# Performance work log

Measured on AMD Instinct MI355X. Metric: run time of the kernel, lower is better.

Reference implementation:

```python
import jax, jax.numpy as jnp
import numpy as np

HEADS = 16
D_MODEL = 1024
HEAD_DIM = D_MODEL // HEADS
NEG = -1e15


def setup_inputs() -> dict:
    key = jax.random.key(0)
    ks = jax.random.split(key, 13)
    B, L = 2, 2048
    scale = 1.0 / np.sqrt(D_MODEL)
    inp = {
        'q': jax.random.normal(ks[0], (B, L, D_MODEL), jnp.float32),
        'k': jax.random.normal(ks[1], (B, L, D_MODEL), jnp.float32),
        'v': jax.random.normal(ks[2], (B, L, D_MODEL), jnp.float32),
        'mask': jax.random.randint(ks[3], (B, 1, 1, L), 0, 2, jnp.int32),
        'Wq': jax.random.normal(ks[4], (D_MODEL, D_MODEL), jnp.float32) * scale,
        'bq': jax.random.normal(ks[5], (D_MODEL,), jnp.float32) * scale,
        'Wk': jax.random.normal(ks[6], (D_MODEL, D_MODEL), jnp.float32) * scale,
        'bk': jax.random.normal(ks[7], (D_MODEL,), jnp.float32) * scale,
        'Wv': jax.random.normal(ks[8], (D_MODEL, D_MODEL), jnp.float32) * scale,
        'bv': jax.random.normal(ks[9], (D_MODEL,), jnp.float32) * scale,
        'Wo': jax.random.normal(ks[10], (D_MODEL, D_MODEL), jnp.float32) * scale,
        'bo': jax.random.normal(ks[11], (D_MODEL,), jnp.float32) * scale,
    }
    return inp


def _split_heads(x):
    B, L, _ = x.shape
    return x.reshape(B, L, HEADS, HEAD_DIM).transpose(0, 2, 1, 3)  # [B,H,L,Dh]


def reference(q, k, v, mask, Wq, bq, Wk, bk, Wv, bv, Wo, bo):
    B, L, _ = q.shape
    # torch Linear: y = x @ W.T + b
    qh = _split_heads(q @ Wq.T + bq)
    kh = _split_heads(k @ Wk.T + bk)
    vh = _split_heads(v @ Wv.T + bv)
    scores = jnp.einsum('bhqd,bhkd->bhqk', qh, kh) / jnp.sqrt(jnp.float32(HEAD_DIM))
    scores = scores + mask.astype(scores.dtype) * NEG
    weights = jax.nn.softmax(scores, axis=-1)
    attn = jnp.einsum('bhqk,bhkd->bhqd', weights, vh)  # [B,H,L,Dh]
    attn = attn.transpose(0, 2, 1, 3).reshape(B, L, D_MODEL)
    return attn @ Wo.T + bo
```

## Files before the change

kernel.cpp:

```cpp
#include <hip/hip_runtime.h>
#include <stdint.h>

typedef __bf16 bf16;
typedef __attribute__((ext_vector_type(8))) __bf16 bf16x8;
typedef __attribute__((ext_vector_type(4))) float f32x4;

#define SEQ   2048
#define DM    1024
#define NH    16
#define HD    64
#define MROWS 4096

__device__ __forceinline__ void glds16(const bf16* g, bf16* l) {
  __builtin_amdgcn_global_load_lds(
      (__attribute__((address_space(1))) unsigned int*)(g),
      (__attribute__((address_space(3))) unsigned int*)(l),
      16, 0, 0);
}

static __device__ __forceinline__ bf16x8 cvt_f32x8(const float* __restrict__ p) {
  const f32x4 a = *(const f32x4*)p;
  const f32x4 b = *(const f32x4*)(p + 4);
  bf16x8 r;
  r[0] = (bf16)a[0]; r[1] = (bf16)a[1]; r[2] = (bf16)a[2]; r[3] = (bf16)a[3];
  r[4] = (bf16)b[0]; r[5] = (bf16)b[1]; r[6] = (bf16)b[2]; r[7] = (bf16)b[3];
  return r;
}

__global__ void conv_all(
    const float* __restrict__ q, const float* __restrict__ k, const float* __restrict__ v,
    const float* __restrict__ wq, const float* __restrict__ wk,
    const float* __restrict__ wv, const float* __restrict__ wo,
    bf16* __restrict__ dq, bf16* __restrict__ dk, bf16* __restrict__ dv,
    bf16* __restrict__ dwq, bf16* __restrict__ dwk, bf16* __restrict__ dwv,
    bf16* __restrict__ dwo)
{
  const size_t c = (size_t)blockIdx.x * 256 + threadIdx.x;
  const float* s; bf16* d; size_t off;
  if (c < 524288)        { s = q;  d = dq;  off = c; }
  else if (c < 1048576)  { s = k;  d = dk;  off = c - 524288; }
  else if (c < 1572864)  { s = v;  d = dv;  off = c - 1048576; }
  else if (c < 1703936)  { s = wq; d = dwq; off = c - 1572864; }
  else if (c < 1835008)  { s = wk; d = dwk; off = c - 1703936; }
  else if (c < 1966080)  { s = wv; d = dwv; off = c - 1835008; }
  else                   { s = wo; d = dwo; off = c - 1966080; }
  *(bf16x8*)(d + off * 8) = cvt_f32x8(s + off * 8);
}

__global__ __launch_bounds__(256, 4) void proj_qkv(
    const bf16* __restrict__ qb, const bf16* __restrict__ kb, const bf16* __restrict__ vb,
    const bf16* __restrict__ Wqb, const bf16* __restrict__ Wkb, const bf16* __restrict__ Wvb,
    const float* __restrict__ bq, const float* __restrict__ bk, const float* __restrict__ bv,
    bf16* __restrict__ Qh, bf16* __restrict__ Kh, bf16* __restrict__ Vt)
{
  __shared__ __align__(16) bf16 sA[128 * 64];
  __shared__ __align__(16) bf16 sB[128 * 64];

  const int z = blockIdx.z;
  const int o = (int)blockIdx.x + 8 * (int)blockIdx.y;
  const int rt = (o & 7) * 4 + ((o >> 3) & 3);
  const int ot = o >> 5;

  const bf16 *A, *B;
  const float* Bv;
  int m0, n0;
  if (z == 0)      { A = qb;  B = Wqb; Bv = bq; m0 = rt * 128; n0 = ot * 128; }
  else if (z == 1) { A = kb;  B = Wkb; Bv = bk; m0 = rt * 128; n0 = ot * 128; }
  else             { A = Wvb; B = vb;  Bv = bv; m0 = ot * 128; n0 = rt * 128; }

  const int tid  = threadIdx.x;
  const int lane = tid & 63;
  const int wv   = tid >> 6;
  const int quad = lane >> 4;
  const int colx = lane & 15;
  const int rm = (wv >> 1) * 64;
  const int rn = (wv & 1) * 64;

  f32x4 acc[4][4];
#pragma unroll
  for (int mi = 0; mi < 4; ++mi)
#pragma unroll
    for (int ni = 0; ni < 4; ++ni) {
      f32x4 zz = {0.f, 0.f, 0.f, 0.f};
      acc[mi][ni] = zz;
    }

  for (int kt = 0; kt < 16; ++kt) {
    const int k0 = kt * 64;
    __syncthreads();
#pragma unroll
    for (int i = 0; i < 4; ++i) {
      const int f = i * 256 + tid;
      const int row = f >> 3;
      const int cc = (f & 7) ^ (row & 7);
      glds16(A + (size_t)(m0 + row) * DM + k0 + cc * 8, sA + f * 8);
      glds16(B + (size_t)(n0 + row) * DM + k0 + cc * 8, sB + f * 8);
    }
    __syncthreads();

    bf16x8 af[4][2], bfr[4][2];
#pragma unroll
    for (int t4 = 0; t4 < 4; ++t4) {
#pragma unroll
      for (int ks = 0; ks < 2; ++ks) {
        const int ra = rm + t4 * 16 + colx;
        af[t4][ks] = *(const bf16x8*)(sA + ra * 64 + (((ks * 4 + quad) ^ (ra & 7)) * 8));
        const int rb = rn + t4 * 16 + colx;
        bfr[t4][ks] = *(const bf16x8*)(sB + rb * 64 + (((ks * 4 + quad) ^ (rb & 7)) * 8));
      }
    }
#pragma unroll
    for (int mi = 0; mi < 4; ++mi)
#pragma unroll
      for (int ni = 0; ni < 4; ++ni) {
        acc[mi][ni] = __builtin_amdgcn_mfma_f32_16x16x32_bf16(af[mi][0], bfr[ni][0], acc[mi][ni], 0, 0, 0);
        acc[mi][ni] = __builtin_amdgcn_mfma_f32_16x16x32_bf16(af[mi][1], bfr[ni][1], acc[mi][ni], 0, 0, 0);
      }
  }

  if (z == 2) {
#pragma unroll
    for (int mi = 0; mi < 4; ++mi) {
#pragma unroll
      for (int r = 0; r < 4; ++r) {
        const int m = m0 + rm + mi * 16 + quad * 4 + r;
        const float bias = Bv[m];
        const int hh = m >> 6, d = m & 63;
#pragma unroll
        for (int ni = 0; ni < 4; ++ni) {
          const int n = n0 + rn + ni * 16 + colx;
          const int b = n >> 11, l = n & 2047;
          const int lb = l >> 7, li = l & 127;
          const int perm = (li & 15) * 8 + ((li >> 4) & 7);
          Vt[(((size_t)(b * NH + hh) * HD + d) * SEQ) + lb * 128 + perm] =
              (bf16)(acc[mi][ni][r] + bias);
        }
      }
    }
  } else {
    bf16* Out = (z == 0) ? Qh : Kh;
    const float scale = (z == 0) ? 0.18033688f : 1.0f;
#pragma unroll
    for (int ni = 0; ni < 4; ++ni) {
      const int n = n0 + rn + ni * 16 + colx;
      const float bias = Bv[n];
#pragma unroll
      for (int mi = 0; mi < 4; ++mi) {
#pragma unroll
        for (int r = 0; r < 4; ++r) {
          const int m = m0 + rm + mi * 16 + quad * 4 + r;
          const float v = (acc[mi][ni][r] + bias) * scale;
          const int b = m >> 11, l = m & 2047, hh = n >> 6, d = n & 63;
          Out[((size_t)(b * NH + hh) * SEQ + l) * HD + d] = (bf16)v;
        }
      }
    }
  }
}

__global__ __launch_bounds__(256, 4) void proj_out(
    const bf16* __restrict__ At, const bf16* __restrict__ Wob,
    const float* __restrict__ bo, float* __restrict__ Out)
{
  __shared__ __align__(16) bf16 sA[128 * 64];
  __shared__ __align__(16) bf16 sB[128 * 64];

  const int o = (int)blockIdx.x + 8 * (int)blockIdx.y;
  const int m0 = ((o & 7) * 4 + ((o >> 3) & 3)) * 128;
  const int n0 = (o >> 5) * 128;

  const int tid  = threadIdx.x;
  const int lane = tid & 63;
  const int wv   = tid >> 6;
  const int quad = lane >> 4;
  const int colx = lane & 15;
  const int rm = (wv >> 1) * 64;
  const int rn = (wv & 1) * 64;

  f32x4 acc[4][4];
#pragma unroll
  for (int mi = 0; mi < 4; ++mi)
#pragma unroll
    for (int ni = 0; ni < 4; ++ni) {
      f32x4 zz = {0.f, 0.f, 0.f, 0.f};
      acc[mi][ni] = zz;
    }

  for (int kt = 0; kt < 16; ++kt) {
    const int k0 = kt * 64;
    __syncthreads();
#pragma unroll
    for (int i = 0; i < 4; ++i) {
      const int f = i * 256 + tid;
      const int row = f >> 3;
      const int cc = (f & 7) ^ (row & 7);
      glds16(At  + (size_t)(m0 + row) * DM + k0 + cc * 8, sA + f * 8);
      glds16(Wob + (size_t)(n0 + row) * DM + k0 + cc * 8, sB + f * 8);
    }
    __syncthreads();

    bf16x8 af[4][2], bfr[4][2];
#pragma unroll
    for (int t4 = 0; t4 < 4; ++t4) {
#pragma unroll
      for (int ks = 0; ks < 2; ++ks) {
        const int ra = rm + t4 * 16 + colx;
        af[t4][ks] = *(const bf16x8*)(sA + ra * 64 + (((ks * 4 + quad) ^ (ra & 7)) * 8));
        const int rb = rn + t4 * 16 + colx;
        bfr[t4][ks] = *(const bf16x8*)(sB + rb * 64 + (((ks * 4 + quad) ^ (rb & 7)) * 8));
      }
    }
#pragma unroll
    for (int mi = 0; mi < 4; ++mi)
#pragma unroll
      for (int ni = 0; ni < 4; ++ni) {
        acc[mi][ni] = __builtin_amdgcn_mfma_f32_16x16x32_bf16(af[mi][0], bfr[ni][0], acc[mi][ni], 0, 0, 0);
        acc[mi][ni] = __builtin_amdgcn_mfma_f32_16x16x32_bf16(af[mi][1], bfr[ni][1], acc[mi][ni], 0, 0, 0);
      }
  }

#pragma unroll
  for (int ni = 0; ni < 4; ++ni) {
    const int n = n0 + rn + ni * 16 + colx;
    const float bias = bo[n];
#pragma unroll
    for (int mi = 0; mi < 4; ++mi) {
#pragma unroll
      for (int r = 0; r < 4; ++r) {
        const int m = m0 + rm + mi * 16 + quad * 4 + r;
        Out[(size_t)m * DM + n] = acc[mi][ni][r] + bias;
      }
    }
  }
}

__global__ __launch_bounds__(256, 2) void attn_kernel(
    const bf16* __restrict__ Qh, const bf16* __restrict__ Kh, const bf16* __restrict__ Vt,
    const int* __restrict__ mask, bf16* __restrict__ At)
{
  __shared__ __align__(16) bf16 sK[128 * 64];
  __shared__ __align__(16) bf16 sVt[80 * 128];
  __shared__ __align__(16) bf16 sP[4][32 * 128];

  const int tid  = threadIdx.x;
  const int lane = tid & 63;
  const int wv   = tid >> 6;
  const int quad = lane >> 4;
  const int colx = lane & 15;
  const int bh = blockIdx.y;
  const int b  = bh >> 4;
  const int h  = bh & 15;
  const int q0 = blockIdx.x * 128;
  const size_t base  = (size_t)bh * SEQ * HD;
  const size_t baseV = (size_t)bh * HD * SEQ;

  {
    const int row = 64 + (tid >> 4);
    const float val = (row == 64) ? 1.0f : 0.0f;
    bf16x8 vv;
#pragma unroll
    for (int j = 0; j < 8; ++j) vv[j] = (bf16)val;
    *(bf16x8*)(sVt + row * 128 + (tid & 15) * 8) = vv;
  }

  bf16x8 stK[4], stV[4];
  int mk[8];

  auto loadkv = [&](int K0) {
#pragma unroll
    for (int i = 0; i < 4; ++i) {
      const int f = i * 256 + tid;
      const int kr = f >> 3;
      const int ck = (f & 7) ^ (kr & 7);
      stK[i] = *(const bf16x8*)(Kh + base + (size_t)(K0 + kr) * HD + ck * 8);
      const int dr = f >> 4;
      const int cv = (f & 15) ^ (dr & 15);
      stV[i] = *(const bf16x8*)(Vt + baseV + (size_t)dr * SEQ + K0 + cv * 8);
    }
#pragma unroll
    for (int nt = 0; nt < 8; ++nt)
      mk[nt] = mask[b * SEQ + K0 + nt * 16 + colx];
  };

  loadkv(0);

  bf16x8 qf[2][2];
#pragma unroll
  for (int half = 0; half < 2; ++half) {
    const int qrow = q0 + wv * 32 + half * 16 + colx;
    qf[half][0] = *(const bf16x8*)(Qh + base + (size_t)qrow * HD + quad * 8);
    qf[half][1] = *(const bf16x8*)(Qh + base + (size_t)qrow * HD + 32 + quad * 8);
  }

  f32x4 o[2][5];
#pragma unroll
  for (int half = 0; half < 2; ++half)
#pragma unroll
    for (int dt = 0; dt < 5; ++dt) {
      f32x4 zz = {0.f, 0.f, 0.f, 0.f};
      o[half][dt] = zz;
    }
  bf16* sPw = &sP[wv][0];

  for (int kc = 0; kc < 16; ++kc) {
    __syncthreads();
#pragma unroll
    for (int i = 0; i < 4; ++i) {
      const int f = i * 256 + tid;
      *(bf16x8*)(sK  + f * 8) = stK[i];
      *(bf16x8*)(sVt + f * 8) = stV[i];
    }
    float mreg[8];
#pragma unroll
    for (int nt = 0; nt < 8; ++nt)
      mreg[nt] = (mk[nt] ? -1e30f : 0.0f) - 23.0830917f;
    if (kc < 15) loadkv((kc + 1) * 128);
    __syncthreads();

#pragma unroll
    for (int half = 0; half < 2; ++half) {
      f32x4 s8[8];
      __builtin_amdgcn_s_setprio(1);
#pragma unroll
      for (int nt = 0; nt < 8; ++nt) {
        f32x4 s = {0.f, 0.f, 0.f, 0.f};
        const int krow = nt * 16 + colx;
#pragma unroll
        for (int ks = 0; ks < 2; ++ks) {
          const bf16x8 kf = *(const bf16x8*)(sK + krow * 64 + (((ks * 4 + quad) ^ (krow & 7)) * 8));
          s = __builtin_amdgcn_mfma_f32_16x16x32_bf16(qf[half][ks], kf, s, 0, 0, 0);
        }
        s8[nt] = s;
      }
      __builtin_amdgcn_s_setprio(0);
#pragma unroll
      for (int r = 0; r < 4; ++r) {
        bf16x8 pk;
#pragma unroll
        for (int nt = 0; nt < 8; ++nt)
          pk[nt] = (bf16)__builtin_amdgcn_exp2f(s8[nt][r] + mreg[nt]);
        const int row = half * 16 + quad * 4 + r;
        *(bf16x8*)(sPw + row * 128 + ((colx ^ (row & 15)) * 8)) = pk;
      }
    }

    __builtin_amdgcn_s_setprio(1);
#pragma unroll
    for (int ks = 0; ks < 4; ++ks) {
      const int ch = ((ks * 4 + quad) ^ colx) * 8;
      const bf16x8 pf0 = *(const bf16x8*)(sPw + colx * 128 + ch);
      const bf16x8 pf1 = *(const bf16x8*)(sPw + (16 + colx) * 128 + ch);
#pragma unroll
      for (int dt = 0; dt < 5; ++dt) {
        const int drow = (dt < 4) ? (dt * 16 + colx) : (64 + colx);
        const bf16x8 vf = *(const bf16x8*)(sVt + drow * 128 + ch);
        o[0][dt] = __builtin_amdgcn_mfma_f32_16x16x32_bf16(pf0, vf, o[0][dt], 0, 0, 0);
        o[1][dt] = __builtin_amdgcn_mfma_f32_16x16x32_bf16(pf1, vf, o[1][dt], 0, 0, 0);
      }
    }
    __builtin_amdgcn_s_setprio(0);
  }

#pragma unroll
  for (int half = 0; half < 2; ++half) {
#pragma unroll
    for (int r = 0; r < 4; ++r) {
      const float lsum = __shfl(o[half][4][r], (lane & 48));
      const float inv = 1.0f / lsum;
      const int q = q0 + wv * 32 + half * 16 + quad * 4 + r;
#pragma unroll
      for (int dt = 0; dt < 4; ++dt) {
        At[((size_t)(b * SEQ + q)) * DM + h * HD + dt * 16 + colx] =
            (bf16)(o[half][dt][r] * inv);
      }
    }
  }
}

extern "C" void kernel_launch(void* const* d_in, const int* in_sizes, int n_in,
                              void* d_out, int out_size, void* d_ws, size_t ws_size,
                              hipStream_t stream) {
  (void)in_sizes; (void)n_in; (void)out_size; (void)ws_size;
  const float* q    = (const float*)d_in[0];
  const float* k    = (const float*)d_in[1];
  const float* v    = (const float*)d_in[2];
  const int*   mask = (const int*)d_in[3];
  const float* Wq   = (const float*)d_in[4];
  const float* bq   = (const float*)d_in[5];
  const float* Wk   = (const float*)d_in[6];
  const float* bk   = (const float*)d_in[7];
  const float* Wv   = (const float*)d_in[8];
  const float* bv   = (const float*)d_in[9];
  const float* Wo   = (const float*)d_in[10];
  const float* bo   = (const float*)d_in[11];
  float* out = (float*)d_out;

  const size_t T = (size_t)MROWS * DM;
  const size_t WT = (size_t)DM * DM;
  bf16* ws  = (bf16*)d_ws;
  bf16* qb  = ws;
  bf16* kb  = qb + T;
  bf16* vb  = kb + T;
  bf16* Wqb = vb + T;
  bf16* Wkb = Wqb + WT;
  bf16* Wvb = Wkb + WT;
  bf16* Wob = Wvb + WT;
  bf16* Qh  = Wob + WT;
  bf16* Kh  = Qh + T;
  bf16* Vt  = Kh + T;
  bf16* At  = qb;

  dim3 blk(256);
  conv_all<<<8192, blk, 0, stream>>>(q, k, v, Wq, Wk, Wv, Wo,
                                     qb, kb, vb, Wqb, Wkb, Wvb, Wob);
  proj_qkv<<<dim3(8, 32, 3), blk, 0, stream>>>(qb, kb, vb, Wqb, Wkb, Wvb,
                                               bq, bk, bv, Qh, Kh, Vt);
  attn_kernel<<<dim3(16, 32), blk, 0, stream>>>(Qh, Kh, Vt, mask, At);
  proj_out<<<dim3(8, 32), blk, 0, stream>>>(At, Wob, bo, out);
}
```

Baseline: 212.9 us.

## Double-buffer K/V via direct global-to-LDS loads and compute row sums with shuffles

The attention kernel now loads K and V tiles straight into a double-buffered LDS area with global_load_lds, instead of staging them through registers and storing to a single buffer. The next tile's load is issued before computing on the current one, which removes one barrier per iteration. Softmax denominators are now summed in fp32 with cross-lane shuffles instead of an extra ones-row MFMA column, the P buffer is halved by processing one half at a time, and the grid order is swapped so blocks with the same head run together. The cost is more LDS per block, which may limit occupancy, and extra shuffle instructions.

```diff
diff --git a/kernel.cpp b/kernel.cpp
--- a/kernel.cpp
+++ b/kernel.cpp
@@ -238,51 +238,40 @@
     const bf16* __restrict__ Qh, const bf16* __restrict__ Kh, const bf16* __restrict__ Vt,
     const int* __restrict__ mask, bf16* __restrict__ At)
 {
-  __shared__ __align__(16) bf16 sK[128 * 64];
-  __shared__ __align__(16) bf16 sVt[80 * 128];
-  __shared__ __align__(16) bf16 sP[4][32 * 128];
+  __shared__ __align__(16) bf16 sK[2][128 * 64];
+  __shared__ __align__(16) bf16 sV[2][64 * 128];
+  __shared__ __align__(16) bf16 sP[4][16 * 128];
 
   const int tid  = threadIdx.x;
   const int lane = tid & 63;
   const int wv   = tid >> 6;
   const int quad = lane >> 4;
   const int colx = lane & 15;
-  const int bh = blockIdx.y;
+  const int bh = blockIdx.x;
   const int b  = bh >> 4;
   const int h  = bh & 15;
-  const int q0 = blockIdx.x * 128;
+  const int q0 = blockIdx.y * 128;
   const size_t base  = (size_t)bh * SEQ * HD;
   const size_t baseV = (size_t)bh * HD * SEQ;
 
-  {
-    const int row = 64 + (tid >> 4);
-    const float val = (row == 64) ? 1.0f : 0.0f;
-    bf16x8 vv;
-#pragma unroll
-    for (int j = 0; j < 8; ++j) vv[j] = (bf16)val;
-    *(bf16x8*)(sVt + row * 128 + (tid & 15) * 8) = vv;
-  }
-
-  bf16x8 stK[4], stV[4];
-  int mk[8];
-
-  auto loadkv = [&](int K0) {
+  auto issue = [&](int K0, bf16* dK, bf16* dV) {
 #pragma unroll
     for (int i = 0; i < 4; ++i) {
       const int f = i * 256 + tid;
       const int kr = f >> 3;
       const int ck = (f & 7) ^ (kr & 7);
-      stK[i] = *(const bf16x8*)(Kh + base + (size_t)(K0 + kr) * HD + ck * 8);
+      glds16(Kh + base + (size_t)(K0 + kr) * HD + ck * 8, dK + f * 8);
       const int dr = f >> 4;
       const int cv = (f & 15) ^ (dr & 15);
-      stV[i] = *(const bf16x8*)(Vt + baseV + (size_t)dr * SEQ + K0 + cv * 8);
-    }
-#pragma unroll
-    for (int nt = 0; nt < 8; ++nt)
-      mk[nt] = mask[b * SEQ + K0 + nt * 16 + colx];
+      glds16(Vt + baseV + (size_t)dr * SEQ + K0 + cv * 8, dV + f * 8);
+    }
   };
 
-  loadkv(0);
+  int mk[8], mkn[8];
+  issue(0, sK[0], sV[0]);
+#pragma unroll
+  for (int nt = 0; nt < 8; ++nt)
+    mk[nt] = mask[b * SEQ + nt * 16 + colx];
 
   bf16x8 qf[2][2];
 #pragma unroll
@@ -292,30 +281,34 @@
     qf[half][1] = *(const bf16x8*)(Qh + base + (size_t)qrow * HD + 32 + quad * 8);
   }
 
-  f32x4 o[2][5];
+  f32x4 o[2][4];
+  float osum[2][4];
 #pragma unroll
   for (int half = 0; half < 2; ++half)
 #pragma unroll
-    for (int dt = 0; dt < 5; ++dt) {
+    for (int dt = 0; dt < 4; ++dt) {
       f32x4 zz = {0.f, 0.f, 0.f, 0.f};
       o[half][dt] = zz;
+      osum[half][dt] = 0.f;
     }
   bf16* sPw = &sP[wv][0];
 
+  __syncthreads();
+
   for (int kc = 0; kc < 16; ++kc) {
-    __syncthreads();
-#pragma unroll
-    for (int i = 0; i < 4; ++i) {
-      const int f = i * 256 + tid;
-      *(bf16x8*)(sK  + f * 8) = stK[i];
-      *(bf16x8*)(sVt + f * 8) = stV[i];
+    const int cur = kc & 1;
+    bf16* cK = &sK[cur][0];
+    bf16* cV = &sV[cur][0];
+    if (kc < 15) {
+      issue((kc + 1) * 128, &sK[cur ^ 1][0], &sV[cur ^ 1][0]);
+#pragma unroll
+      for (int nt = 0; nt < 8; ++nt)
+        mkn[nt] = mask[b * SEQ + (kc + 1) * 128 + nt * 16 + colx];
     }
     float mreg[8];
 #pragma unroll
     for (int nt = 0; nt < 8; ++nt)
       mreg[nt] = (mk[nt] ? -1e30f : 0.0f) - 23.0830917f;
-    if (kc < 15) loadkv((kc + 1) * 128);
-    __syncthreads();
 
 #pragma unroll
     for (int half = 0; half < 2; ++half) {
@@ -327,46 +320,63 @@
         const int krow = nt * 16 + colx;
 #pragma unroll
         for (int ks = 0; ks < 2; ++ks) {
-          const bf16x8 kf = *(const bf16x8*)(sK + krow * 64 + (((ks * 4 + quad) ^ (krow & 7)) * 8));
+          const bf16x8 kf = *(const bf16x8*)(cK + krow * 64 + (((ks * 4 + quad) ^ (krow & 7)) * 8));
           s = __builtin_amdgcn_mfma_f32_16x16x32_bf16(qf[half][ks], kf, s, 0, 0, 0);
         }
         s8[nt] = s;
       }
       __builtin_amdgcn_s_setprio(0);
+
+      float rs[4];
 #pragma unroll
       for (int r = 0; r < 4; ++r) {
         bf16x8 pk;
-#pragma unroll
-        for (int nt = 0; nt < 8; ++nt)
-          pk[nt] = (bf16)__builtin_amdgcn_exp2f(s8[nt][r] + mreg[nt]);
-        const int row = half * 16 + quad * 4 + r;
-        *(bf16x8*)(sPw + row * 128 + ((colx ^ (row & 15)) * 8)) = pk;
-      }
-    }
-
-    __builtin_amdgcn_s_setprio(1);
-#pragma unroll
-    for (int ks = 0; ks < 4; ++ks) {
-      const int ch = ((ks * 4 + quad) ^ colx) * 8;
-      const bf16x8 pf0 = *(const bf16x8*)(sPw + colx * 128 + ch);
-      const bf16x8 pf1 = *(const bf16x8*)(sPw + (16 + colx) * 128 + ch);
-#pragma unroll
-      for (int dt = 0; dt < 5; ++dt) {
-        const int drow = (dt < 4) ? (dt * 16 + colx) : (64 + colx);
-        const bf16x8 vf = *(const bf16x8*)(sVt + drow * 128 + ch);
-        o[0][dt] = __builtin_amdgcn_mfma_f32_16x16x32_bf16(pf0, vf, o[0][dt], 0, 0, 0);
-        o[1][dt] = __builtin_amdgcn_mfma_f32_16x16x32_bf16(pf1, vf, o[1][dt], 0, 0, 0);
-      }
-    }
-    __builtin_amdgcn_s_setprio(0);
+        float rsum = 0.f;
+#pragma unroll
+        for (int nt = 0; nt < 8; ++nt) {
+          const float e = __builtin_amdgcn_exp2f(s8[nt][r] + mreg[nt]);
+          pk[nt] = (bf16)e;
+          rsum += e;
+        }
+        const int row = quad * 4 + r;
+        *(bf16x8*)(sPw + row * 128 + ((colx ^ row) * 8)) = pk;
+        rs[r] = rsum;
+      }
+#pragma unroll
+      for (int r = 0; r < 4; ++r) {
+        rs[r] += __shfl_xor(rs[r], 1);
+        rs[r] += __shfl_xor(rs[r], 2);
+        rs[r] += __shfl_xor(rs[r], 4);
+        rs[r] += __shfl_xor(rs[r], 8);
+        osum[half][r] += rs[r];
+      }
+
+      __builtin_amdgcn_s_setprio(1);
+#pragma unroll
+      for (int ks = 0; ks < 4; ++ks) {
+        const int ch = ((ks * 4 + quad) ^ colx) * 8;
+        const bf16x8 pf = *(const bf16x8*)(sPw + colx * 128 + ch);
+#pragma unroll
+        for (int dt = 0; dt < 4; ++dt) {
+          const bf16x8 vf = *(const bf16x8*)(cV + (dt * 16 + colx) * 128 + ch);
+          o[half][dt] = __builtin_amdgcn_mfma_f32_16x16x32_bf16(pf, vf, o[half][dt], 0, 0, 0);
+        }
+      }
+      __builtin_amdgcn_s_setprio(0);
+    }
+
+    if (kc < 15) {
+#pragma unroll
+      for (int nt = 0; nt < 8; ++nt) mk[nt] = mkn[nt];
+    }
+    __syncthreads();
   }
 
 #pragma unroll
   for (int half = 0; half < 2; ++half) {
 #pragma unroll
     for (int r = 0; r < 4; ++r) {
-      const float lsum = __shfl(o[half][4][r], (lane & 48));
-      const float inv = 1.0f / lsum;
+      const float inv = 1.0f / osum[half][r];
       const int q = q0 + wv * 32 + half * 16 + quad * 4 + r;
 #pragma unroll
       for (int dt = 0; dt < 4; ++dt) {
@@ -415,6 +425,6 @@
                                      qb, kb, vb, Wqb, Wkb, Wvb, Wob);
   proj_qkv<<<dim3(8, 32, 3), blk, 0, stream>>>(qb, kb, vb, Wqb, Wkb, Wvb,
                                                bq, bk, bv, Qh, Kh, Vt);
-  attn_kernel<<<dim3(16, 32), blk, 0, stream>>>(Qh, Kh, Vt, mask, At);
+  attn_kernel<<<dim3(32, 16), blk, 0, stream>>>(Qh, Kh, Vt, mask, At);
   proj_out<<<dim3(8, 32), blk, 0, stream>>>(At, Wob, bo, out);
 }
```

After: 225.4 us. 1.06x slower.
